# Performance work log

Hardware: AMD Instinct MI355X
Metric: run time of the kernel (lower is better)

Reference implementation:

```python
import jax, jax.numpy as jnp
import numpy as np

# ---- constants baked from __init__ (sample_rate=44100, plate_params=None) ----
SR = 44100
K = 1.0 / SR                      # time step
LX = 1.0
FMAX = 10000.0
MAX_OM = FMAX * 2.0 * np.pi
TAU0, TAU1, LOSS_F1 = 6.0, 2.0, 500.0
_OM2 = 2.0 * np.pi * LOSS_F1
_DOMSQ = _OM2 ** 2                # OmDamp1 = 0
ALPHA = 3.0 * np.log(10.0) / _DOMSQ * (_OM2 ** 2 / TAU0)
BETA = 3.0 * np.log(10.0) / _DOMSQ * (1.0 / TAU1 - 1.0 / TAU0)
M_MAX = N_MAX = 80                # 6400 modes
_gm, _gn = np.meshgrid(np.arange(1, M_MAX + 1), np.arange(1, N_MAX + 1), indexing='ij')
M_VEC = jnp.asarray(_gm.reshape(-1), dtype=jnp.float32)
N_VEC = jnp.asarray(_gn.reshape(-1), dtype=jnp.float32)
PI = np.float32(np.pi)


def setup_inputs() -> dict:
    key = jax.random.key(0)
    ks = jax.random.split(key, 6)
    names = ['mu_raw', 'D_over_mu_raw', 'T0_over_mu_raw', 'Ly_raw', 'xo_raw', 'yo_raw']
    inp = {n: jax.random.normal(k, (), dtype=jnp.float32) for n, k in zip(names, ks)}
    inp['num_samples'] = 22050   # duration = 0.5 s at 44100 Hz
    return inp


def reference(mu_raw, D_over_mu_raw, T0_over_mu_raw, Ly_raw, xo_raw, yo_raw, num_samples):
    # physical parameter transforms
    mu = jax.nn.softplus(mu_raw) + 1e-4
    D_over_mu = jax.nn.softplus(D_over_mu_raw) + 1e-4
    T0_over_mu = jax.nn.softplus(T0_over_mu_raw) + 1e-4
    Ly = 1.1 + (4.0 - 1.1) * ((jnp.tanh(Ly_raw) + 1.0) / 2.0)
    xo = 0.49 * LX + (1.0 - 0.49) * LX * ((jnp.tanh(xo_raw) + 1.0) / 2.0)
    yo = 0.51 * Ly + (1.0 - 0.51) * Ly * ((jnp.tanh(yo_raw) + 1.0) / 2.0)

    xi = 0.335 * LX
    yi = 0.467 * Ly

    # modal frequencies / damping, shape [6400]
    g1 = (M_VEC * PI / LX) ** 2 + (N_VEC * PI / Ly) ** 2
    omega_sq = T0_over_mu * g1 + D_over_mu * g1 * g1
    omega = jnp.sqrt(jax.nn.relu(omega_sq))
    temp = 100.0
    valid = jax.nn.sigmoid((MAX_OM - omega) / temp) * jax.nn.sigmoid((omega - 20.0 * 2.0 * PI) / temp)

    in_w = jnp.cos(xi * PI * M_VEC / LX) * jnp.cos(yi * PI * N_VEC / Ly)
    out_w = jnp.cos(xo * PI * M_VEC / LX) * jnp.cos(yo * PI * N_VEC / Ly)
    sigma = ALPHA + BETA * omega ** 2
    ms = 0.25 * mu * LX * Ly
    P = out_w * in_w * (K ** 2) * jnp.exp(-sigma * K) / ms * valid

    # damped sinusoid bank: [6400 modes, num_samples] grids, summed over modes
    n = jnp.arange(num_samples, dtype=jnp.float32)                  # [T]
    coef = P / (jnp.sin(omega * K) + 1e-8)                          # [M]
    env = jnp.exp(-sigma[:, None] * (n[None, :] * K))               # [M, T]
    sine = jnp.sin((n[None, :] + 1.0) * (omega[:, None] * K))       # [M, T]
    disp = jnp.einsum('m,mt,mt->t', coef, env, sine)                # [T]

    # velocity via first difference (velCalc=True)
    prev = jnp.concatenate([jnp.zeros((1,), dtype=disp.dtype), disp[:-1]])
    ir = (disp - prev) / K

    # peak normalization (normalize=True)
    return ir / (jnp.max(jnp.abs(ir)) + 1e-8)
```

## Files before the change

### kernel.cpp

```cpp
#include <hip/hip_runtime.h>
#include <math.h>

#define PI_D      3.14159265358979323846
#define K_D       (1.0 / 44100.0)
#define MAX_OM_D  (10000.0 * 2.0 * PI_D)
#define LN10      2.30258509299404568402
#define ALPHA_D   (3.0 * LN10 / 6.0)
#define OM2_D     (2.0 * PI_D * 500.0)
#define BETA_D    (3.0 * LN10 / (OM2_D * OM2_D) * (1.0 / 2.0 - 1.0 / 6.0))
#define LOG2E_D   1.44269504088896340736
#define INV2PI_D  0.15915494309189533577

#define NMODES  6400
#define TPB     256
#define NS      6
#define TILE    (TPB * NS)
#define NCHUNK  32
#define CHUNK_M (NMODES / NCHUNK)

#if defined(__has_builtin) && __has_builtin(__builtin_amdgcn_sinf)
#define SIN_REV(x) __builtin_amdgcn_sinf(x)
#else
#define SIN_REV(x) __sinf((x) * 6.28318530717958647692f)
#endif
#if defined(__has_builtin) && __has_builtin(__builtin_amdgcn_cosf)
#define COS_REV(x) __builtin_amdgcn_cosf(x)
#else
#define COS_REV(x) __cosf((x) * 6.28318530717958647692f)
#endif
#if defined(__has_builtin) && __has_builtin(__builtin_amdgcn_exp2f)
#define EXP2F(x) __builtin_amdgcn_exp2f(x)
#else
#define EXP2F(x) exp2f(x)
#endif
#if defined(__has_builtin) && __has_builtin(__builtin_amdgcn_fractf)
#define FRACTF(x) __builtin_amdgcn_fractf(x)
#else
#define FRACTF(x) ((x) - floorf(x))
#endif

__device__ inline double softplus_fast(double x) {
    float xf = (float)x;
    float r = (xf > 0.0f) ? xf + log1pf(__expf(-xf)) : log1pf(__expf(xf));
    return (double)r;
}
__device__ inline float cosrev_d(double x) { return COS_REV((float)(x - floor(x))); }
__device__ inline float sinrev_d(double x) { return SIN_REV((float)(x - floor(x))); }
__device__ inline float sigmoid_f(double x) { return 1.0f / (1.0f + __expf((float)(-x))); }

__global__ void mode_params_kernel(const float* __restrict__ mu_raw,
                                   const float* __restrict__ Dmu_raw,
                                   const float* __restrict__ Tmu_raw,
                                   const float* __restrict__ Ly_raw,
                                   const float* __restrict__ xo_raw,
                                   const float* __restrict__ yo_raw,
                                   double* __restrict__ phase64,
                                   float4* __restrict__ pdA,
                                   float4* __restrict__ pdB,
                                   float* __restrict__ disp,
                                   unsigned int* __restrict__ gmax, int T) {
    int i = blockIdx.x * blockDim.x + threadIdx.x;

    for (int k = i; k < T; k += gridDim.x * blockDim.x) disp[k] = 0.0f;
    if (i == 0) *gmax = 0u;

    if (i >= NMODES) return;

    double mu  = softplus_fast((double)mu_raw[0])  + 1e-4;
    double Dmu = softplus_fast((double)Dmu_raw[0]) + 1e-4;
    double Tmu = softplus_fast((double)Tmu_raw[0]) + 1e-4;
    double Ly  = 1.1 + (4.0 - 1.1) * (((double)tanhf(Ly_raw[0]) + 1.0) * 0.5);
    double xo  = 0.49 + 0.51 * (((double)tanhf(xo_raw[0]) + 1.0) * 0.5);
    double yoL = 0.51 + 0.49 * (((double)tanhf(yo_raw[0]) + 1.0) * 0.5);

    int m = i / 80 + 1, n = i % 80 + 1;
    double md = (double)m, nd = (double)n;
    double invLy = 1.0 / Ly;
    double a  = md * PI_D;
    double b  = nd * PI_D * invLy;
    double g1 = a * a + b * b;
    double omsq  = Tmu * g1 + Dmu * g1 * g1;
    double omega = sqrt(omsq > 0.0 ? omsq : 0.0);

    float valid = sigmoid_f((MAX_OM_D - omega) * 0.01) *
                  sigmoid_f((omega - 40.0 * PI_D) * 0.01);
    float in_w  = cosrev_d(0.1675 * md) * cosrev_d(0.2335 * nd);
    float out_w = cosrev_d(0.5 * xo * md) * cosrev_d(0.5 * yoL * nd);

    double sigma = ALPHA_D + BETA_D * omega * omega;
    double ph64  = omega * K_D * INV2PI_D;
    float envK = __expf((float)(-sigma * K_D));
    float P    = out_w * in_w * (float)(K_D * K_D / (0.25 * mu * Ly)) * envK * valid;
    float coef = P / (sinrev_d(ph64) + 1e-8f);
    float dec2 = (float)(-sigma * K_D * LOG2E_D);

    float r256 = EXP2F(dec2 * 256.0f);
    double p256 = ph64 * 256.0;
    float d256 = (float)(p256 - floor(p256));
    float c1 = 2.0f * r256 * COS_REV(d256);
    float c2 = r256 * r256;

    phase64[i] = ph64;
    pdA[i] = make_float4(coef, dec2, c1, c2);
    pdB[i] = make_float4((float)ph64, d256, r256, 0.0f);
}

__global__ __launch_bounds__(TPB) void synth_kernel(const double* __restrict__ phase64,
                                                    const float4* __restrict__ pdA,
                                                    const float4* __restrict__ pdB,
                                                    float* __restrict__ disp, int T) {
    __shared__ float4 sA[CHUNK_M];
    __shared__ float4 sB[CHUNK_M];
    __shared__ int    s_cnt;

    const int m0 = blockIdx.y * CHUNK_M;
    const int t0 = blockIdx.x * TILE;
    const int tid = threadIdx.x;

    if (tid == 0) s_cnt = 0;
    __syncthreads();

    if (tid < CHUNK_M) {
        float4 p = pdA[m0 + tid];
        float cb = p.x * EXP2F(p.y * (float)t0);
        if (cb != 0.0f) {
            float4 q = pdB[m0 + tid];
            double bd = phase64[m0 + tid] * (double)(t0 + 1);
            float base = (float)(bd - floor(bd));
            int idx = atomicAdd(&s_cnt, 1);
            sA[idx] = make_float4(base, cb, p.z, p.w);
            sB[idx] = make_float4(q.x, q.y, q.z, p.y);
        }
    }
    __syncthreads();
    const int n_act = s_cnt;

    float acc[NS];
    #pragma unroll
    for (int i = 0; i < NS; ++i) acc[i] = 0.0f;
    const float tidf = (float)tid;

    for (int j = 0; j < n_act; ++j) {
        float4 a = sA[j];
        float4 b = sB[j];
        float ang0 = fmaf(b.x, tidf, a.x);
        float s0 = SIN_REV(FRACTF(ang0));
        float s1 = SIN_REV(FRACTF(ang0 + b.y));
        float ce = a.y * EXP2F(b.w * tidf);
        float y0 = ce * s0;
        float y1 = ce * b.z * s1;
        acc[0] += y0;
        acc[1] += y1;
        #pragma unroll
        for (int i = 2; i < NS; ++i) {
            float y2 = fmaf(a.z, y1, -(a.w * y0));
            acc[i] += y2;
            y0 = y1; y1 = y2;
        }
    }
    #pragma unroll
    for (int i = 0; i < NS; ++i) {
        int t = t0 + tid + TPB * i;
        if (t < T) atomicAdd(&disp[t], acc[i]);
    }
}

__global__ void diff_max_kernel(const float* __restrict__ disp,
                                float* __restrict__ out,
                                unsigned int* __restrict__ gmax, int T) {
    __shared__ float s_red[TPB / 64];
    int t = blockIdx.x * blockDim.x + threadIdx.x;
    float v = 0.0f;
    if (t < T) {
        float p = (t > 0) ? disp[t - 1] : 0.0f;
        v = (disp[t] - p) * 44100.0f;
        out[t] = v;
    }
    float lmax = fabsf(v);
    for (int o = 32; o > 0; o >>= 1)
        lmax = fmaxf(lmax, __shfl_down(lmax, o, 64));
    if ((threadIdx.x & 63) == 0) s_red[threadIdx.x >> 6] = lmax;
    __syncthreads();
    if (threadIdx.x == 0) {
        float m0 = fmaxf(fmaxf(s_red[0], s_red[1]), fmaxf(s_red[2], s_red[3]));
        atomicMax(gmax, __float_as_uint(m0));
    }
}

__global__ void normalize_kernel(float* __restrict__ out,
                                 const unsigned int* __restrict__ gmax, int T) {
    int t = blockIdx.x * blockDim.x + threadIdx.x;
    if (t >= T) return;
    out[t] = out[t] / (__uint_as_float(*gmax) + 1e-8f);
}

extern "C" void kernel_launch(void* const* d_in, const int* in_sizes, int n_in,
                              void* d_out, int out_size, void* d_ws, size_t ws_size,
                              hipStream_t stream) {
    const float* mu_raw  = (const float*)d_in[0];
    const float* Dmu_raw = (const float*)d_in[1];
    const float* Tmu_raw = (const float*)d_in[2];
    const float* Ly_raw  = (const float*)d_in[3];
    const float* xo_raw  = (const float*)d_in[4];
    const float* yo_raw  = (const float*)d_in[5];
    float* out = (float*)d_out;
    int T = out_size;
    if (T <= 0) return;

    char* ws = (char*)d_ws;
    double* phase64 = (double*)(ws + 0);
    float4* pdA     = (float4*)(ws + 51200);
    float4* pdB     = (float4*)(ws + 153600);
    unsigned int* gmax = (unsigned int*)(ws + 256000);
    float*  disp    = (float*)(ws + 256256);

    int nb = ((T > NMODES ? T : NMODES) + TPB - 1) / TPB;
    mode_params_kernel<<<nb, TPB, 0, stream>>>(
        mu_raw, Dmu_raw, Tmu_raw, Ly_raw, xo_raw, yo_raw,
        phase64, pdA, pdB, disp, gmax, T);

    dim3 grid((T + TILE - 1) / TILE, NCHUNK);
    synth_kernel<<<grid, TPB, 0, stream>>>(phase64, pdA, pdB, disp, T);

    int nb2 = (T + TPB - 1) / TPB;
    diff_max_kernel<<<nb2, TPB, 0, stream>>>(disp, out, gmax, T);
    normalize_kernel<<<nb2, TPB, 0, stream>>>(out, gmax, T);
}
```

Measured before the change: 96.75 us.

## Compact live modes globally and replace atomic accumulation with per-chunk partial sums

The mode setup kernel now writes only modes with nonzero coefficient into a compacted list via a global atomic counter. The synth kernel splits that compacted list across 64 y-chunks instead of 32 fixed chunks, which balances work when many modes are killed by the validity window. Each block writes its partial sums to a per-chunk row instead of issuing global float atomics, and the diff kernel reduces the 64 rows. This removes the disp zeroing and atomic contention, at the cost of a larger workspace, an extra memset, and a 64-way read reduction per sample.

```diff
diff --git a/kernel.cpp b/kernel.cpp
--- a/kernel.cpp
+++ b/kernel.cpp
@@ -15,8 +15,8 @@
 #define TPB     256
 #define NS      6
 #define TILE    (TPB * NS)
-#define NCHUNK  32
-#define CHUNK_M (NMODES / NCHUNK)
+#define NCHY    64
+#define CHUNK_M (NMODES / NCHY)
 
 #if defined(__has_builtin) && __has_builtin(__builtin_amdgcn_sinf)
 #define SIN_REV(x) __builtin_amdgcn_sinf(x)
@@ -54,16 +54,13 @@
                                    const float* __restrict__ Ly_raw,
                                    const float* __restrict__ xo_raw,
                                    const float* __restrict__ yo_raw,
-                                   double* __restrict__ phase64,
-                                   float4* __restrict__ pdA,
-                                   float4* __restrict__ pdB,
-                                   float* __restrict__ disp,
-                                   unsigned int* __restrict__ gmax, int T) {
+                                   double* __restrict__ cPh,
+                                   float4* __restrict__ cA,
+                                   float4* __restrict__ cB,
+                                   unsigned int* __restrict__ g_cnt,
+                                   unsigned int* __restrict__ gmax) {
     int i = blockIdx.x * blockDim.x + threadIdx.x;
-
-    for (int k = i; k < T; k += gridDim.x * blockDim.x) disp[k] = 0.0f;
     if (i == 0) *gmax = 0u;
-
     if (i >= NMODES) return;
 
     double mu  = softplus_fast((double)mu_raw[0])  + 1e-4;
@@ -94,38 +91,48 @@
     float coef = P / (sinrev_d(ph64) + 1e-8f);
     float dec2 = (float)(-sigma * K_D * LOG2E_D);
 
-    float r256 = EXP2F(dec2 * 256.0f);
-    double p256 = ph64 * 256.0;
-    float d256 = (float)(p256 - floor(p256));
-    float c1 = 2.0f * r256 * COS_REV(d256);
-    float c2 = r256 * r256;
-
-    phase64[i] = ph64;
-    pdA[i] = make_float4(coef, dec2, c1, c2);
-    pdB[i] = make_float4((float)ph64, d256, r256, 0.0f);
-}
-
-__global__ __launch_bounds__(TPB) void synth_kernel(const double* __restrict__ phase64,
-                                                    const float4* __restrict__ pdA,
-                                                    const float4* __restrict__ pdB,
-                                                    float* __restrict__ disp, int T) {
+    if (coef != 0.0f) {
+        float r256 = EXP2F(dec2 * 256.0f);
+        double p256 = ph64 * 256.0;
+        float d256 = (float)(p256 - floor(p256));
+        float c1 = 2.0f * r256 * COS_REV(d256);
+        float c2 = r256 * r256;
+
+        unsigned int idx = atomicAdd(g_cnt, 1u);
+        cPh[idx] = ph64;
+        cA[idx]  = make_float4(coef, dec2, c1, c2);
+        cB[idx]  = make_float4((float)ph64, d256, r256, 0.0f);
+    }
+}
+
+__global__ __launch_bounds__(TPB) void synth_kernel(const double* __restrict__ cPh,
+                                                    const float4* __restrict__ cA,
+                                                    const float4* __restrict__ cB,
+                                                    const unsigned int* __restrict__ g_cnt,
+                                                    float* __restrict__ part,
+                                                    int T, int Tpad) {
     __shared__ float4 sA[CHUNK_M];
     __shared__ float4 sB[CHUNK_M];
     __shared__ int    s_cnt;
 
-    const int m0 = blockIdx.y * CHUNK_M;
     const int t0 = blockIdx.x * TILE;
     const int tid = threadIdx.x;
 
     if (tid == 0) s_cnt = 0;
     __syncthreads();
 
-    if (tid < CHUNK_M) {
-        float4 p = pdA[m0 + tid];
+    const int n_live = (int)*g_cnt;
+    const int chunk  = (n_live + NCHY - 1) / NCHY;
+    const int j0     = blockIdx.y * chunk;
+    const int cnt    = min(chunk, n_live - j0);
+
+    if (tid < cnt) {
+        int j = j0 + tid;
+        float4 p = cA[j];
         float cb = p.x * EXP2F(p.y * (float)t0);
         if (cb != 0.0f) {
-            float4 q = pdB[m0 + tid];
-            double bd = phase64[m0 + tid] * (double)(t0 + 1);
+            float4 q = cB[j];
+            double bd = cPh[j] * (double)(t0 + 1);
             float base = (float)(bd - floor(bd));
             int idx = atomicAdd(&s_cnt, 1);
             sA[idx] = make_float4(base, cb, p.z, p.w);
@@ -158,22 +165,43 @@
             y0 = y1; y1 = y2;
         }
     }
+
+    float* row = part + (size_t)blockIdx.y * (size_t)Tpad + t0;
     #pragma unroll
     for (int i = 0; i < NS; ++i) {
-        int t = t0 + tid + TPB * i;
-        if (t < T) atomicAdd(&disp[t], acc[i]);
-    }
-}
-
-__global__ void diff_max_kernel(const float* __restrict__ disp,
+        int tt = tid + TPB * i;
+        if (t0 + tt < T) row[tt] = acc[i];
+    }
+}
+
+__global__ void diff_max_kernel(const float* __restrict__ part,
                                 float* __restrict__ out,
-                                unsigned int* __restrict__ gmax, int T) {
+                                unsigned int* __restrict__ gmax, int T, int Tpad) {
+    __shared__ float ssum[TPB + 1];
     __shared__ float s_red[TPB / 64];
     int t = blockIdx.x * blockDim.x + threadIdx.x;
+
+    float s = 0.0f;
+    if (t < T) {
+        #pragma unroll 8
+        for (int y = 0; y < NCHY; ++y) s += part[(size_t)y * (size_t)Tpad + t];
+    }
+    ssum[threadIdx.x + 1] = s;
+    if (threadIdx.x == 0) {
+        float sp = 0.0f;
+        int tp = t - 1;
+        if (tp >= 0 && tp < T) {
+            #pragma unroll 8
+            for (int y = 0; y < NCHY; ++y) sp += part[(size_t)y * (size_t)Tpad + tp];
+        }
+        ssum[0] = sp;
+    }
+    __syncthreads();
+
     float v = 0.0f;
     if (t < T) {
-        float p = (t > 0) ? disp[t - 1] : 0.0f;
-        v = (disp[t] - p) * 44100.0f;
+        float p = (t > 0) ? ssum[threadIdx.x] : 0.0f;
+        v = (s - p) * 44100.0f;
         out[t] = v;
     }
     float lmax = fabsf(v);
@@ -208,21 +236,27 @@
     if (T <= 0) return;
 
     char* ws = (char*)d_ws;
-    double* phase64 = (double*)(ws + 0);
-    float4* pdA     = (float4*)(ws + 51200);
-    float4* pdB     = (float4*)(ws + 153600);
-    unsigned int* gmax = (unsigned int*)(ws + 256000);
-    float*  disp    = (float*)(ws + 256256);
-
-    int nb = ((T > NMODES ? T : NMODES) + TPB - 1) / TPB;
-    mode_params_kernel<<<nb, TPB, 0, stream>>>(
+    unsigned int* g_cnt = (unsigned int*)(ws + 0);
+    unsigned int* gmax  = (unsigned int*)(ws + 4);
+    double* cPh = (double*)(ws + 256);
+    float4* cA  = (float4*)(ws + 256 + 51200);
+    float4* cB  = (float4*)(ws + 256 + 153600);
+    float*  part = (float*)(ws + 262144);
+
+    int ntx  = (T + TILE - 1) / TILE;
+    int Tpad = ntx * TILE;
+
+    hipMemsetAsync(g_cnt, 0, sizeof(unsigned int), stream);
+
+    int nb1 = (NMODES + TPB - 1) / TPB;
+    mode_params_kernel<<<nb1, TPB, 0, stream>>>(
         mu_raw, Dmu_raw, Tmu_raw, Ly_raw, xo_raw, yo_raw,
-        phase64, pdA, pdB, disp, gmax, T);
-
-    dim3 grid((T + TILE - 1) / TILE, NCHUNK);
-    synth_kernel<<<grid, TPB, 0, stream>>>(phase64, pdA, pdB, disp, T);
+        cPh, cA, cB, g_cnt, gmax);
+
+    dim3 grid(ntx, NCHY);
+    synth_kernel<<<grid, TPB, 0, stream>>>(cPh, cA, cB, g_cnt, part, T, Tpad);
 
     int nb2 = (T + TPB - 1) / TPB;
-    diff_max_kernel<<<nb2, TPB, 0, stream>>>(disp, out, gmax, T);
+    diff_max_kernel<<<nb2, TPB, 0, stream>>>(part, out, gmax, T, Tpad);
     normalize_kernel<<<nb2, TPB, 0, stream>>>(out, gmax, T);
 }
```

After: 105.7 us. +9.3%, slower.
